# Performance work log

Measured on AMD Instinct MI355X. Metric: run time of the kernel, lower is better.

Reference implementation:

```python
import jax, jax.numpy as jnp
import numpy as np

B, S, H, E, I, TOP_K = 2, 1024, 1024, 8, 1408, 2
W_SCALE = 0.02


def setup_inputs() -> dict:
    key = jax.random.key(0)
    ks = jax.random.split(key, 5)
    return {
        "hidden_states": jax.random.normal(ks[0], (B, S, H), dtype=jnp.float32),
        "router_weight": jax.random.normal(ks[1], (H, E), dtype=jnp.float32) * W_SCALE,
        "gate_proj": jax.random.normal(ks[2], (E, H, I), dtype=jnp.float32) * W_SCALE,
        "up_proj": jax.random.normal(ks[3], (E, H, I), dtype=jnp.float32) * W_SCALE,
        "down_proj": jax.random.normal(ks[4], (E, I, H), dtype=jnp.float32) * W_SCALE,
        "gate_bias": jnp.zeros((E, I), dtype=jnp.float32),
        "up_bias": jnp.zeros((E, I), dtype=jnp.float32),
        "down_bias": jnp.zeros((E, H), dtype=jnp.float32),
        "top_k": TOP_K,
    }


def reference(hidden_states, router_weight, gate_proj, up_proj, down_proj,
              gate_bias, up_bias, down_bias, top_k):
    b, s, h = hidden_states.shape
    e = gate_proj.shape[0]
    x = hidden_states.reshape(-1, h)              # [T, H], T = b*s
    t = x.shape[0]

    # --- RouterAdapter: MoEGate top-k then scatter into dense scores [T, E] ---
    logits = x @ router_weight                    # [T, E]
    probs = jax.nn.softmax(logits, axis=-1)
    topk_w, topk_idx = jax.lax.top_k(probs, top_k)  # [T, k]
    topk_w = topk_w / jnp.sum(topk_w, axis=-1, keepdims=True)  # norm_topk_prob
    scores = jnp.zeros((t, e), dtype=topk_w.dtype)
    scores = scores.at[jnp.arange(t)[:, None], topk_idx].set(topk_w)

    # --- StackedExperts.sparse_forward (dense equivalent of sparse matmuls) ---
    g = jnp.einsum('th,ehi->tei', x, gate_proj) + gate_bias[None]  # [T, E, I]
    u = jnp.einsum('th,ehi->tei', x, up_proj) + up_bias[None]      # [T, E, I]
    act = jax.nn.silu(g) * u                       # ACTIVATION_DEEPSEEK
    d = jnp.einsum('tei,eih->teh', act, down_proj) + down_bias[None]  # [T, E, H]

    # combine per-expert outputs with router scores (non-routed scores are 0,
    # matching the sparse matmul's zero blocks)
    y = jnp.einsum('teh,te->th', d, scores)
    return y.reshape(b, s, h)
```

## Files before the change

### kernel.cpp

```cpp
#include <hip/hip_runtime.h>

#define T_TOK 2048
#define HDIM  1024
#define NEXP  8
#define IDIM  1408

#define BM 128
#define BN 64
#define BK 32
#define MT_SLOTS 16
#define GU_NT 22
#define DN_NT 16
#define DK_HALF 704

#define GU_BLOCKS   (8 * GU_NT * MT_SLOTS)
#define PREP_RTR    512
#define PREP_GRID   (PREP_RTR + 16 * 176)
#define GUWD_GRID   (GU_BLOCKS + 8 * 176)

#define SM_A    0
#define SM_G    8192
#define SM_U    12288
#define SM_GR   16384
#define SM_OR   16896
#define SM_SZ   17408

typedef __attribute__((ext_vector_type(8))) short bf16x8;
typedef __attribute__((ext_vector_type(4))) float f32x4;

static __device__ __forceinline__ unsigned short f2bf(float f) {
    union { float f; unsigned u; } a; a.f = f;
    return (unsigned short)((a.u + 0x7fffu + ((a.u >> 16) & 1u)) >> 16);
}

#define GLOAD16(gsrc, ldst)                                                  \
    __builtin_amdgcn_global_load_lds(                                        \
        (const __attribute__((address_space(1))) unsigned int*)(gsrc),       \
        (__attribute__((address_space(3))) unsigned int*)(ldst), 16, 0, 0)

__global__ __launch_bounds__(256) void prep_kernel(
    const float* __restrict__ x,
    const float* __restrict__ rw,
    const float* __restrict__ gw,
    const float* __restrict__ uw,
    int*   __restrict__ sel,
    float* __restrict__ w1arr,
    unsigned short* __restrict__ xb,
    unsigned short* __restrict__ gwt,
    unsigned short* __restrict__ uwt)
{
    __shared__ __align__(16) char smem[32768];
    const int tid = threadIdx.x;
    const int bx  = blockIdx.x;

    if (bx < PREP_RTR) {
        float (*rwT)[HDIM] = (float (*)[HDIM])smem;
#pragma unroll
        for (int p = 0; p < 4; ++p) {
            const int h = tid + 256 * p;
            const float4 a = *(const float4*)(rw + (size_t)h * 8);
            const float4 b = *(const float4*)(rw + (size_t)h * 8 + 4);
            rwT[0][h] = a.x; rwT[1][h] = a.y; rwT[2][h] = a.z; rwT[3][h] = a.w;
            rwT[4][h] = b.x; rwT[5][h] = b.y; rwT[6][h] = b.z; rwT[7][h] = b.w;
        }
        __syncthreads();

        const int t    = bx * 4 + (tid >> 6);
        const int lane = tid & 63;
        if (t >= T_TOK) return;

        float xr[16];
        const float* xp = x + (size_t)t * HDIM;
#pragma unroll
        for (int i = 0; i < 16; ++i) xr[i] = xp[lane + 64 * i];

        unsigned short* xbp = xb + (size_t)t * HDIM;
#pragma unroll
        for (int i = 0; i < 16; ++i) xbp[lane + 64 * i] = f2bf(xr[i]);

        double logits[NEXP];
#pragma unroll
        for (int e = 0; e < NEXP; ++e) {
            double s = 0.0;
#pragma unroll
            for (int i = 0; i < 16; ++i)
                s += (double)xr[i] * (double)rwT[e][lane + 64 * i];
#pragma unroll
            for (int off = 32; off > 0; off >>= 1)
                s += __shfl_down(s, off, 64);
            logits[e] = s;
        }

        if (lane == 0) {
            int e1 = 0;
            for (int e = 1; e < NEXP; ++e) if (logits[e] > logits[e1]) e1 = e;
            int e2 = -1;
            for (int e = 0; e < NEXP; ++e) {
                if (e == e1) continue;
                if (e2 < 0 || logits[e] > logits[e2]) e2 = e;
            }
            const double w1 = 1.0 / (1.0 + exp(logits[e2] - logits[e1]));
            sel[t]   = e1 | (e2 << 8);
            w1arr[t] = (float)w1;
        }
    } else {
        const int idx = bx - PREP_RTR;
        const int z   = idx / 176;
        const int b   = idx - z * 176;
        const int e   = z & 7;
        const float* src = (z < 8 ? gw : uw) + (size_t)e * HDIM * IDIM;
        unsigned short* dst =
            (z < 8 ? gwt : uwt) + (size_t)e * (size_t)IDIM * HDIM;
        const int nb = b % 11, kb = b / 11;
        const int k0 = kb * 64, n0 = nb * 128;

        unsigned short (*tb)[66] = (unsigned short (*)[66])smem;

        const int lk = tid >> 5;
        const int ln = (tid & 31) * 4;
#pragma unroll
        for (int r = 0; r < 8; ++r) {
            const int k = r * 8 + lk;
            const float4 v =
                *(const float4*)(src + (size_t)(k0 + k) * IDIM + n0 + ln);
            tb[ln + 0][k] = f2bf(v.x);
            tb[ln + 1][k] = f2bf(v.y);
            tb[ln + 2][k] = f2bf(v.z);
            tb[ln + 3][k] = f2bf(v.w);
        }
        __syncthreads();

        const int wn = tid >> 3;
        const int wk = (tid & 7) * 8;
#pragma unroll
        for (int p = 0; p < 4; ++p) {
            const int n = p * 32 + wn;
            const unsigned* rp = (const unsigned*)&tb[n][wk];
            uint4 o;
            o.x = rp[0]; o.y = rp[1]; o.z = rp[2]; o.w = rp[3];
            *(uint4*)(dst + (size_t)(n0 + n) * HDIM + k0 + wk) = o;
        }
    }
}

__global__ __launch_bounds__(1024) void router_scatter_kernel(
    const int* __restrict__ sel, const float* __restrict__ w1arr,
    int* __restrict__ counts,
    int* __restrict__ tok_list, float* __restrict__ wgt_list,
    int* __restrict__ row_list)
{
    __shared__ int cnt[NEXP];
    const int tid = threadIdx.x;
    if (tid < NEXP) cnt[tid] = 0;
    __syncthreads();
    for (int t = tid; t < T_TOK; t += 1024) {
        const int s  = sel[t];
        const int e1 = s & 255, e2 = s >> 8;
        const float w1 = w1arr[t];
        const int p1 = atomicAdd(&cnt[e1], 1);
        tok_list[e1 * T_TOK + p1] = t;
        wgt_list[e1 * T_TOK + p1] = w1;
        row_list[e1 * T_TOK + p1] = 2 * t;
        const int p2 = atomicAdd(&cnt[e2], 1);
        tok_list[e2 * T_TOK + p2] = t;
        wgt_list[e2 * T_TOK + p2] = 1.0f - w1;
        row_list[e2 * T_TOK + p2] = 2 * t + 1;
    }
    __syncthreads();
    if (tid < NEXP) counts[tid] = cnt[tid];
}

__global__ __launch_bounds__(256) void gateup_wd_kernel(
    const unsigned short* __restrict__ xb,
    const unsigned short* __restrict__ gwt,
    const unsigned short* __restrict__ uwt,
    const float* __restrict__ gb, const float* __restrict__ ub,
    const int* __restrict__ counts,
    const int* __restrict__ tok_list,
    const int* __restrict__ row_list,
    unsigned short* __restrict__ act,
    const float* __restrict__ dw,
    unsigned short* __restrict__ dwt)
{
    __shared__ __align__(16) char smem[SM_SZ];
    const int tid  = threadIdx.x;
    const int flat = blockIdx.x;

    if (flat >= GU_BLOCKS) {
        const int idx = flat - GU_BLOCKS;
        const int e   = idx / 176;
        const int b   = idx - e * 176;
        const float* src = dw + (size_t)e * IDIM * HDIM;
        unsigned short* dst = dwt + (size_t)e * (size_t)HDIM * IDIM;
        const int nb = b & 7, kb = b >> 3;
        const int k0 = kb * 64, n0 = nb * 128;

        unsigned short (*tb)[66] = (unsigned short (*)[66])smem;

        const int lk = tid >> 5;
        const int ln = (tid & 31) * 4;
#pragma unroll
        for (int r = 0; r < 8; ++r) {
            const int k = r * 8 + lk;
            const float4 v =
                *(const float4*)(src + (size_t)(k0 + k) * HDIM + n0 + ln);
            tb[ln + 0][k] = f2bf(v.x);
            tb[ln + 1][k] = f2bf(v.y);
            tb[ln + 2][k] = f2bf(v.z);
            tb[ln + 3][k] = f2bf(v.w);
        }
        __syncthreads();

        const int wn = tid >> 3;
        const int wk = (tid & 7) * 8;
#pragma unroll
        for (int p = 0; p < 4; ++p) {
            const int n = p * 32 + wn;
            const unsigned* rp = (const unsigned*)&tb[n][wk];
            uint4 o;
            o.x = rp[0]; o.y = rp[1]; o.z = rp[2]; o.w = rp[3];
            *(uint4*)(dst + (size_t)(n0 + n) * IDIM + k0 + wk) = o;
        }
        return;
    }

    unsigned short (*As)[32] = (unsigned short (*)[32])(smem + SM_A);
    unsigned short (*Bg)[32] = (unsigned short (*)[32])(smem + SM_G);
    unsigned short (*Bu)[32] = (unsigned short (*)[32])(smem + SM_U);
    int* gr_lds = (int*)(smem + SM_GR);
    int* or_lds = (int*)(smem + SM_OR);

    const int xcd  = flat & 7;
    const int q    = flat >> 3;
    const int mt   = q & 15;
    const int slot = q >> 4;
    const int P    = slot * 8 + xcd;
    const int e    = P / GU_NT;
    const int nt   = P % GU_NT;
    const int n_e  = counts[e];
    const int m0   = mt * BM;
    if (m0 >= n_e) return;
    const int n0 = nt * BN;

    const unsigned short* gwp = gwt + (size_t)e * IDIM * HDIM;
    const unsigned short* uwp = uwt + (size_t)e * IDIM * HDIM;
    const float* gbp = gb + (size_t)e * IDIM;
    const float* ubp = ub + (size_t)e * IDIM;

    const int base = e * T_TOK;
    if (tid < BM) {
        const int m = m0 + tid;
        int g = -1, o = -1;
        if (m < n_e) { g = tok_list[base + m]; o = row_list[base + m]; }
        gr_lds[tid] = g; or_lds[tid] = o;
    }
    __syncthreads();

    const int wv = tid >> 6, lane = tid & 63;
    const int lr = lane >> 2;
    const int lc = (lane & 3) * 8;

    const int r0 = 32 * wv + lr;
    const int r1 = 32 * wv + 16 + lr;
    int a0 = gr_lds[r0]; if (a0 < 0) a0 = 0;
    int a1 = gr_lds[r1]; if (a1 < 0) a1 = 0;
    const unsigned short* apA0 = xb + (size_t)a0 * HDIM + lc;
    const unsigned short* apA1 = xb + (size_t)a1 * HDIM + lc;
    unsigned short* dA0 = &As[32 * wv][0];
    unsigned short* dA1 = &As[32 * wv + 16][0];
    const unsigned short* gpB = gwp + (size_t)(n0 + 16 * wv + lr) * HDIM + lc;
    const unsigned short* upB = uwp + (size_t)(n0 + 16 * wv + lr) * HDIM + lc;
    unsigned short* dBg = &Bg[16 * wv][0];
    unsigned short* dBu = &Bu[16 * wv][0];

    const int wm = (wv & 1) * 64, wn = (wv >> 1) * 32;
    const int l16 = lane & 15, quad = lane >> 4;

    f32x4 accg[4][2], accu[4][2];
    const f32x4 zero = {0.0f, 0.0f, 0.0f, 0.0f};
#pragma unroll
    for (int i = 0; i < 4; ++i)
#pragma unroll
        for (int j = 0; j < 2; ++j) { accg[i][j] = zero; accu[i][j] = zero; }

    for (int k0 = 0; k0 < HDIM; k0 += BK) {
        __syncthreads();
        GLOAD16(apA0 + k0, dA0);
        GLOAD16(apA1 + k0, dA1);
        GLOAD16(gpB + k0, dBg);
        GLOAD16(upB + k0, dBu);
        __syncthreads();

        bf16x8 af[4], bgf[2], buf_[2];
#pragma unroll
        for (int i = 0; i < 4; ++i)
            af[i] = *(const bf16x8*)&As[wm + i * 16 + l16][quad * 8];
#pragma unroll
        for (int j = 0; j < 2; ++j) {
            bgf[j]  = *(const bf16x8*)&Bg[wn + j * 16 + l16][quad * 8];
            buf_[j] = *(const bf16x8*)&Bu[wn + j * 16 + l16][quad * 8];
        }
#pragma unroll
        for (int i = 0; i < 4; ++i)
#pragma unroll
            for (int j = 0; j < 2; ++j) {
                accg[i][j] = __builtin_amdgcn_mfma_f32_16x16x32_bf16(
                    af[i], bgf[j], accg[i][j], 0, 0, 0);
                accu[i][j] = __builtin_amdgcn_mfma_f32_16x16x32_bf16(
                    af[i], buf_[j], accu[i][j], 0, 0, 0);
            }
    }

#pragma unroll
    for (int j = 0; j < 2; ++j) {
        const int nl = n0 + wn + j * 16 + l16;
        const float gbv = gbp[nl];
        const float ubv = ubp[nl];
#pragma unroll
        for (int i = 0; i < 4; ++i) {
#pragma unroll
            for (int ii = 0; ii < 4; ++ii) {
                const int ml = wm + i * 16 + quad * 4 + ii;
                const int orow = or_lds[ml];
                if (orow >= 0) {
                    const float g = accg[i][j][ii] + gbv;
                    const float uu = accu[i][j][ii] + ubv;
                    act[(size_t)orow * IDIM + nl] =
                        f2bf(g * uu / (1.0f + __expf(-g)));
                }
            }
        }
    }
}

__global__ __launch_bounds__(256) void down_kernel(
    const unsigned short* __restrict__ act,
    const unsigned short* __restrict__ dwt,
    const float* __restrict__ db,
    const int* __restrict__ counts,
    const float* __restrict__ wgt_list,
    const int* __restrict__ row_list,
    float* __restrict__ y2)
{
    const int flat = blockIdx.x;
    const int xcd  = flat & 7;
    const int q    = flat >> 3;
    const int mt   = q & 15;
    const int slot = q >> 4;
    const int P    = slot * 8 + xcd;
    const int sk   = P & 1;
    const int en   = P >> 1;
    const int e    = en >> 4;
    const int nt   = en & 15;
    const int n_e  = counts[e];
    const int m0   = mt * BM;
    if (m0 >= n_e) return;
    const int n0 = nt * BN;
    const int ks = sk * DK_HALF;
    float* y2s = y2 + (size_t)sk * 2 * T_TOK * HDIM;

    const unsigned short* dwp = dwt + (size_t)e * HDIM * IDIM;
    const float* dbp = db + (size_t)e * HDIM;

    __shared__ unsigned short As[BM][32];
    __shared__ unsigned short Bs[BN][32];
    __shared__ int   r_lds[BM];
    __shared__ float w_lds[BM];

    const int tid = threadIdx.x;
    const int base = e * T_TOK;
    if (tid < BM) {
        const int m = m0 + tid;
        int r = -1; float w = 0.0f;
        if (m < n_e) { r = row_list[base + m]; w = wgt_list[base + m]; }
        r_lds[tid] = r; w_lds[tid] = w;
    }
    __syncthreads();

    const int wv = tid >> 6, lane = tid & 63;
    const int lr = lane >> 2;
    const int lc = (lane & 3) * 8;

    const int r0 = 32 * wv + lr;
    const int r1 = 32 * wv + 16 + lr;
    int a0 = r_lds[r0]; if (a0 < 0) a0 = 0;
    int a1 = r_lds[r1]; if (a1 < 0) a1 = 0;
    const unsigned short* apA0 = act + (size_t)a0 * IDIM + ks + lc;
    const unsigned short* apA1 = act + (size_t)a1 * IDIM + ks + lc;
    unsigned short* dA0 = &As[32 * wv][0];
    unsigned short* dA1 = &As[32 * wv + 16][0];
    const unsigned short* bpB =
        dwp + (size_t)(n0 + 16 * wv + lr) * IDIM + ks + lc;
    unsigned short* dB = &Bs[16 * wv][0];

    const int wm = (wv & 1) * 64, wn = (wv >> 1) * 32;
    const int l16 = lane & 15, quad = lane >> 4;

    f32x4 acc[4][2];
    const f32x4 zero = {0.0f, 0.0f, 0.0f, 0.0f};
#pragma unroll
    for (int i = 0; i < 4; ++i)
#pragma unroll
        for (int j = 0; j < 2; ++j) acc[i][j] = zero;

    for (int k0 = 0; k0 < DK_HALF; k0 += BK) {
        __syncthreads();
        GLOAD16(apA0 + k0, dA0);
        GLOAD16(apA1 + k0, dA1);
        GLOAD16(bpB + k0, dB);
        __syncthreads();

        bf16x8 af[4], bfr[2];
#pragma unroll
        for (int i = 0; i < 4; ++i)
            af[i] = *(const bf16x8*)&As[wm + i * 16 + l16][quad * 8];
#pragma unroll
        for (int j = 0; j < 2; ++j)
            bfr[j] = *(const bf16x8*)&Bs[wn + j * 16 + l16][quad * 8];
#pragma unroll
        for (int i = 0; i < 4; ++i)
#pragma unroll
            for (int j = 0; j < 2; ++j)
                acc[i][j] = __builtin_amdgcn_mfma_f32_16x16x32_bf16(
                    af[i], bfr[j], acc[i][j], 0, 0, 0);
    }

#pragma unroll
    for (int j = 0; j < 2; ++j) {
        const int nl = n0 + wn + j * 16 + l16;
        const float bv = (sk == 0) ? dbp[nl] : 0.0f;
#pragma unroll
        for (int i = 0; i < 4; ++i) {
#pragma unroll
            for (int ii = 0; ii < 4; ++ii) {
                const int ml = wm + i * 16 + quad * 4 + ii;
                const int rr = r_lds[ml];
                if (rr >= 0)
                    y2s[(size_t)rr * HDIM + nl] = w_lds[ml] * (acc[i][j][ii] + bv);
            }
        }
    }
}

__global__ __launch_bounds__(256) void combine_kernel(
    const float* __restrict__ y2, float* __restrict__ out)
{
    const int idx = (blockIdx.x * 256 + threadIdx.x) * 4;
    const int t = idx >> 10;
    const int h = idx & 1023;
    const float* y2b = y2 + (size_t)2 * T_TOK * HDIM;
    const float4 a0 = *(const float4*)(y2  + ((size_t)2 * t) * HDIM + h);
    const float4 a1 = *(const float4*)(y2  + ((size_t)2 * t + 1) * HDIM + h);
    const float4 b0 = *(const float4*)(y2b + ((size_t)2 * t) * HDIM + h);
    const float4 b1 = *(const float4*)(y2b + ((size_t)2 * t + 1) * HDIM + h);
    float4 o;
    o.x = a0.x + a1.x + b0.x + b1.x;
    o.y = a0.y + a1.y + b0.y + b1.y;
    o.z = a0.z + a1.z + b0.z + b1.z;
    o.w = a0.w + a1.w + b0.w + b1.w;
    *(float4*)(out + idx) = o;
}

extern "C" void kernel_launch(void* const* d_in, const int* in_sizes, int n_in,
                              void* d_out, int out_size, void* d_ws, size_t ws_size,
                              hipStream_t stream)
{
    const float* x      = (const float*)d_in[0];
    const float* rw     = (const float*)d_in[1];
    const float* gate_w = (const float*)d_in[2];
    const float* up_w   = (const float*)d_in[3];
    const float* down_w = (const float*)d_in[4];
    const float* gate_b = (const float*)d_in[5];
    const float* up_b   = (const float*)d_in[6];
    const float* down_b = (const float*)d_in[7];
    float* out = (float*)d_out;

    char* ws = (char*)d_ws;
    size_t off = 0;
    int*   counts   = (int*)(ws + off);  off += 256;
    int*   tok_list = (int*)(ws + off);  off += 65536;
    float* wgt_list = (float*)(ws + off); off += 65536;
    int*   row_list = (int*)(ws + off);  off += 65536;
    int*   sel      = (int*)(ws + off);  off += T_TOK * 4;
    float* w1arr    = (float*)(ws + off); off += T_TOK * 4;
    unsigned short* x_bf = (unsigned short*)(ws + off); off += (size_t)T_TOK * HDIM * 2;
    unsigned short* act  = (unsigned short*)(ws + off); off += (size_t)2 * T_TOK * IDIM * 2;
    unsigned short* dwt  = (unsigned short*)(ws + off); off += (size_t)NEXP * IDIM * HDIM * 2;
    unsigned short* gwt  = (unsigned short*)(ws + off); off += (size_t)NEXP * IDIM * HDIM * 2;
    unsigned short* uwt  = (unsigned short*)(ws + off);
    float* y2 = (float*)gwt;

    prep_kernel<<<PREP_GRID, 256, 0, stream>>>(
        x, rw, gate_w, up_w, sel, w1arr, x_bf, gwt, uwt);

    router_scatter_kernel<<<1, 1024, 0, stream>>>(
        sel, w1arr, counts, tok_list, wgt_list, row_list);

    gateup_wd_kernel<<<GUWD_GRID, 256, 0, stream>>>(
        x_bf, gwt, uwt, gate_b, up_b, counts, tok_list, row_list, act,
        down_w, dwt);

    down_kernel<<<2 * 8 * DN_NT * MT_SLOTS, 256, 0, stream>>>(
        act, dwt, down_b, counts, wgt_list, row_list, y2);

    combine_kernel<<<(T_TOK * HDIM / 4) / 256, 256, 0, stream>>>(y2, out);
}
```

Before: 273.4 us.

## Double-buffer LDS tiles in gate/up and down expert GEMM loops

Both expert GEMM loops (the fused gate/up projection and the split-K down projection) now use two LDS buffers per operand. The next K-tile's global_load_lds is issued before the MFMA work on the current tile, so memory latency can overlap with compute, and there is one barrier per tile instead of two. The cost is roughly double the shared memory per block (about 33 KB in the gate/up path), which may lower how many blocks fit per CU.

```diff
diff --git a/kernel.cpp b/kernel.cpp
--- a/kernel.cpp
+++ b/kernel.cpp
@@ -18,12 +18,15 @@
 #define PREP_GRID   (PREP_RTR + 16 * 176)
 #define GUWD_GRID   (GU_BLOCKS + 8 * 176)
 
-#define SM_A    0
-#define SM_G    8192
-#define SM_U    12288
-#define SM_GR   16384
-#define SM_OR   16896
-#define SM_SZ   17408
+#define SM_A0   0
+#define SM_A1   8192
+#define SM_G0   16384
+#define SM_G1   20480
+#define SM_U0   24576
+#define SM_U1   28672
+#define SM_GR   32768
+#define SM_OR   33280
+#define SM_SZ   33792
 
 typedef __attribute__((ext_vector_type(8))) short bf16x8;
 typedef __attribute__((ext_vector_type(4))) float f32x4;
@@ -37,6 +40,62 @@
     __builtin_amdgcn_global_load_lds(                                        \
         (const __attribute__((address_space(1))) unsigned int*)(gsrc),       \
         (__attribute__((address_space(3))) unsigned int*)(ldst), 16, 0, 0)
+
+static __device__ __forceinline__ void gu_stage(
+    const unsigned short* apA0, const unsigned short* apA1,
+    const unsigned short* gpB, const unsigned short* upB, int k,
+    unsigned short* dA0, unsigned short* dA1,
+    unsigned short* dBg, unsigned short* dBu)
+{
+    GLOAD16(apA0 + k, dA0);
+    GLOAD16(apA1 + k, dA1);
+    GLOAD16(gpB + k, dBg);
+    GLOAD16(upB + k, dBu);
+}
+
+static __device__ __forceinline__ void gu_mma(
+    const unsigned short* As, const unsigned short* Bg,
+    const unsigned short* Bu, int wm, int wn, int l16, int quad,
+    f32x4 (*accg)[2], f32x4 (*accu)[2])
+{
+    bf16x8 af[4], bgf[2], bu_[2];
+#pragma unroll
+    for (int i = 0; i < 4; ++i)
+        af[i] = *(const bf16x8*)(As + (wm + i * 16 + l16) * 32 + quad * 8);
+#pragma unroll
+    for (int j = 0; j < 2; ++j) {
+        bgf[j] = *(const bf16x8*)(Bg + (wn + j * 16 + l16) * 32 + quad * 8);
+        bu_[j] = *(const bf16x8*)(Bu + (wn + j * 16 + l16) * 32 + quad * 8);
+    }
+#pragma unroll
+    for (int i = 0; i < 4; ++i)
+#pragma unroll
+        for (int j = 0; j < 2; ++j) {
+            accg[i][j] = __builtin_amdgcn_mfma_f32_16x16x32_bf16(
+                af[i], bgf[j], accg[i][j], 0, 0, 0);
+            accu[i][j] = __builtin_amdgcn_mfma_f32_16x16x32_bf16(
+                af[i], bu_[j], accu[i][j], 0, 0, 0);
+        }
+}
+
+static __device__ __forceinline__ void dn_mma(
+    const unsigned short* As, const unsigned short* Bs,
+    int wm, int wn, int l16, int quad, f32x4 (*acc)[2])
+{
+    bf16x8 af[4], bfr[2];
+#pragma unroll
+    for (int i = 0; i < 4; ++i)
+        af[i] = *(const bf16x8*)(As + (wm + i * 16 + l16) * 32 + quad * 8);
+#pragma unroll
+    for (int j = 0; j < 2; ++j)
+        bfr[j] = *(const bf16x8*)(Bs + (wn + j * 16 + l16) * 32 + quad * 8);
+#pragma unroll
+    for (int i = 0; i < 4; ++i)
+#pragma unroll
+        for (int j = 0; j < 2; ++j)
+            acc[i][j] = __builtin_amdgcn_mfma_f32_16x16x32_bf16(
+                af[i], bfr[j], acc[i][j], 0, 0, 0);
+}
 
 __global__ __launch_bounds__(256) void prep_kernel(
     const float* __restrict__ x,
@@ -224,9 +283,6 @@
         return;
     }
 
-    unsigned short (*As)[32] = (unsigned short (*)[32])(smem + SM_A);
-    unsigned short (*Bg)[32] = (unsigned short (*)[32])(smem + SM_G);
-    unsigned short (*Bu)[32] = (unsigned short (*)[32])(smem + SM_U);
     int* gr_lds = (int*)(smem + SM_GR);
     int* or_lds = (int*)(smem + SM_OR);
 
@@ -261,17 +317,23 @@
     const int lc = (lane & 3) * 8;
 
     const int r0 = 32 * wv + lr;
-    const int r1 = 32 * wv + 16 + lr;
+    const int r1 = r0 + 16;
     int a0 = gr_lds[r0]; if (a0 < 0) a0 = 0;
     int a1 = gr_lds[r1]; if (a1 < 0) a1 = 0;
     const unsigned short* apA0 = xb + (size_t)a0 * HDIM + lc;
     const unsigned short* apA1 = xb + (size_t)a1 * HDIM + lc;
-    unsigned short* dA0 = &As[32 * wv][0];
-    unsigned short* dA1 = &As[32 * wv + 16][0];
     const unsigned short* gpB = gwp + (size_t)(n0 + 16 * wv + lr) * HDIM + lc;
     const unsigned short* upB = uwp + (size_t)(n0 + 16 * wv + lr) * HDIM + lc;
-    unsigned short* dBg = &Bg[16 * wv][0];
-    unsigned short* dBu = &Bu[16 * wv][0];
+
+    const int oA0 = (32 * wv) * 32;
+    const int oA1 = (32 * wv + 16) * 32;
+    const int oB  = (16 * wv) * 32;
+    unsigned short* A0b = (unsigned short*)(smem + SM_A0);
+    unsigned short* A1b = (unsigned short*)(smem + SM_A1);
+    unsigned short* G0b = (unsigned short*)(smem + SM_G0);
+    unsigned short* G1b = (unsigned short*)(smem + SM_G1);
+    unsigned short* U0b = (unsigned short*)(smem + SM_U0);
+    unsigned short* U1b = (unsigned short*)(smem + SM_U1);
 
     const int wm = (wv & 1) * 64, wn = (wv >> 1) * 32;
     const int l16 = lane & 15, quad = lane >> 4;
@@ -283,32 +345,20 @@
 #pragma unroll
         for (int j = 0; j < 2; ++j) { accg[i][j] = zero; accu[i][j] = zero; }
 
-    for (int k0 = 0; k0 < HDIM; k0 += BK) {
-        __syncthreads();
-        GLOAD16(apA0 + k0, dA0);
-        GLOAD16(apA1 + k0, dA1);
-        GLOAD16(gpB + k0, dBg);
-        GLOAD16(upB + k0, dBu);
-        __syncthreads();
-
-        bf16x8 af[4], bgf[2], buf_[2];
-#pragma unroll
-        for (int i = 0; i < 4; ++i)
-            af[i] = *(const bf16x8*)&As[wm + i * 16 + l16][quad * 8];
-#pragma unroll
-        for (int j = 0; j < 2; ++j) {
-            bgf[j]  = *(const bf16x8*)&Bg[wn + j * 16 + l16][quad * 8];
-            buf_[j] = *(const bf16x8*)&Bu[wn + j * 16 + l16][quad * 8];
-        }
-#pragma unroll
-        for (int i = 0; i < 4; ++i)
-#pragma unroll
-            for (int j = 0; j < 2; ++j) {
-                accg[i][j] = __builtin_amdgcn_mfma_f32_16x16x32_bf16(
-                    af[i], bgf[j], accg[i][j], 0, 0, 0);
-                accu[i][j] = __builtin_amdgcn_mfma_f32_16x16x32_bf16(
-                    af[i], buf_[j], accu[i][j], 0, 0, 0);
-            }
+    gu_stage(apA0, apA1, gpB, upB, 0,
+             A0b + oA0, A0b + oA1, G0b + oB, U0b + oB);
+    __syncthreads();
+
+    for (int k0 = 0; k0 < HDIM; k0 += 2 * BK) {
+        gu_stage(apA0, apA1, gpB, upB, k0 + BK,
+                 A1b + oA0, A1b + oA1, G1b + oB, U1b + oB);
+        gu_mma(A0b, G0b, U0b, wm, wn, l16, quad, accg, accu);
+        __syncthreads();
+        if (k0 + 2 * BK < HDIM)
+            gu_stage(apA0, apA1, gpB, upB, k0 + 2 * BK,
+                     A0b + oA0, A0b + oA1, G0b + oB, U0b + oB);
+        gu_mma(A1b, G1b, U1b, wm, wn, l16, quad, accg, accu);
+        __syncthreads();
     }
 
 #pragma unroll
@@ -362,8 +412,8 @@
     const unsigned short* dwp = dwt + (size_t)e * HDIM * IDIM;
     const float* dbp = db + (size_t)e * HDIM;
 
-    __shared__ unsigned short As[BM][32];
-    __shared__ unsigned short Bs[BN][32];
+    __shared__ unsigned short As0[BM][32], As1[BM][32];
+    __shared__ unsigned short Bs0[BN][32], Bs1[BN][32];
     __shared__ int   r_lds[BM];
     __shared__ float w_lds[BM];
 
@@ -382,16 +432,19 @@
     const int lc = (lane & 3) * 8;
 
     const int r0 = 32 * wv + lr;
-    const int r1 = 32 * wv + 16 + lr;
+    const int r1 = r0 + 16;
     int a0 = r_lds[r0]; if (a0 < 0) a0 = 0;
     int a1 = r_lds[r1]; if (a1 < 0) a1 = 0;
     const unsigned short* apA0 = act + (size_t)a0 * IDIM + ks + lc;
     const unsigned short* apA1 = act + (size_t)a1 * IDIM + ks + lc;
-    unsigned short* dA0 = &As[32 * wv][0];
-    unsigned short* dA1 = &As[32 * wv + 16][0];
     const unsigned short* bpB =
         dwp + (size_t)(n0 + 16 * wv + lr) * IDIM + ks + lc;
-    unsigned short* dB = &Bs[16 * wv][0];
+    unsigned short* dA0_0 = &As0[32 * wv][0];
+    unsigned short* dA1_0 = &As0[32 * wv + 16][0];
+    unsigned short* dA0_1 = &As1[32 * wv][0];
+    unsigned short* dA1_1 = &As1[32 * wv + 16][0];
+    unsigned short* dB_0  = &Bs0[16 * wv][0];
+    unsigned short* dB_1  = &Bs1[16 * wv][0];
 
     const int wm = (wv & 1) * 64, wn = (wv >> 1) * 32;
     const int l16 = lane & 15, quad = lane >> 4;
@@ -403,26 +456,24 @@
 #pragma unroll
         for (int j = 0; j < 2; ++j) acc[i][j] = zero;
 
-    for (int k0 = 0; k0 < DK_HALF; k0 += BK) {
-        __syncthreads();
-        GLOAD16(apA0 + k0, dA0);
-        GLOAD16(apA1 + k0, dA1);
-        GLOAD16(bpB + k0, dB);
-        __syncthreads();
-
-        bf16x8 af[4], bfr[2];
-#pragma unroll
-        for (int i = 0; i < 4; ++i)
-            af[i] = *(const bf16x8*)&As[wm + i * 16 + l16][quad * 8];
-#pragma unroll
-        for (int j = 0; j < 2; ++j)
-            bfr[j] = *(const bf16x8*)&Bs[wn + j * 16 + l16][quad * 8];
-#pragma unroll
-        for (int i = 0; i < 4; ++i)
-#pragma unroll
-            for (int j = 0; j < 2; ++j)
-                acc[i][j] = __builtin_amdgcn_mfma_f32_16x16x32_bf16(
-                    af[i], bfr[j], acc[i][j], 0, 0, 0);
+    GLOAD16(apA0, dA0_0);
+    GLOAD16(apA1, dA1_0);
+    GLOAD16(bpB, dB_0);
+    __syncthreads();
+
+    for (int k0 = 0; k0 < DK_HALF; k0 += 2 * BK) {
+        GLOAD16(apA0 + k0 + BK, dA0_1);
+        GLOAD16(apA1 + k0 + BK, dA1_1);
+        GLOAD16(bpB + k0 + BK, dB_1);
+        dn_mma(&As0[0][0], &Bs0[0][0], wm, wn, l16, quad, acc);
+        __syncthreads();
+        if (k0 + 2 * BK < DK_HALF) {
+            GLOAD16(apA0 + k0 + 2 * BK, dA0_0);
+            GLOAD16(apA1 + k0 + 2 * BK, dA1_0);
+            GLOAD16(bpB + k0 + 2 * BK, dB_0);
+        }
+        dn_mma(&As1[0][0], &Bs1[0][0], wm, wn, l16, quad, acc);
+        __syncthreads();
     }
 
 #pragma unroll
```

Result: no change. 271.5 us (-0.7%).
